# Optimization experiments

Hardware: AMD Instinct MI355X
Metric: run time of the kernel (lower is better)

The kernel has to match this reference:

```python
import jax, jax.numpy as jnp
import numpy as np

OMEGA = 10.0
SIGMA = 10.0
HID = 256
IN_DIM = 3
OUT_DIM = 3


def gabor(x, W, b):
    # torch.nn.Linear: lin = x @ W.T + b
    lin = x @ W.T + b
    # exp(1j*omega*lin - (sigma*lin)**2).real == cos(omega*lin) * exp(-(sigma*lin)**2)
    return jnp.cos(OMEGA * lin) * jnp.exp(-jnp.square(SIGMA * lin))


def _linear_init(key, out_dim, in_dim):
    kw, kb = jax.random.split(key)
    bound = 1.0 / np.sqrt(in_dim)
    W = jax.random.uniform(kw, (out_dim, in_dim), jnp.float32, -bound, bound)
    b = jax.random.uniform(kb, (out_dim,), jnp.float32, -bound, bound)
    return W, b


def setup_inputs() -> dict:
    key = jax.random.key(0)
    keys = jax.random.split(key, 7)
    N = 262144
    x = jax.random.uniform(keys[0], (N, IN_DIM), jnp.float32)
    W0, b0 = _linear_init(keys[1], HID, IN_DIM)
    W1, b1 = _linear_init(keys[2], HID, HID)
    W2, b2 = _linear_init(keys[3], HID, HID)
    W3, b3 = _linear_init(keys[4], HID, HID + IN_DIM)  # skip-concat layer
    W4, b4 = _linear_init(keys[5], HID, HID)
    Wf, bf = _linear_init(keys[6], OUT_DIM, HID)
    return {"x": x, "W0": W0, "b0": b0, "W1": W1, "b1": b1, "W2": W2,
            "b2": b2, "W3": W3, "b3": b3, "W4": W4, "b4": b4,
            "Wf": Wf, "bf": bf}


def reference(x, W0, b0, W1, b1, W2, b2, W3, b3, W4, b4, Wf, bf):
    x_in = x
    h = gabor(x, W0, b0)          # net[0]
    h = gabor(h, W1, b1)          # net[1]
    h = gabor(h, W2, b2)          # net[2]
    h = jnp.concatenate([h, x_in], axis=-1)  # skip before net[3]
    h = gabor(h, W3, b3)          # net[3]
    h = gabor(h, W4, b4)          # net[4]
    return h @ Wf.T + bf          # final linear
```

## Files before the change

### kernel.cpp

```cpp
#include <hip/hip_runtime.h>

typedef _Float16 f16x8 __attribute__((ext_vector_type(8)));
typedef _Float16 f16x4 __attribute__((ext_vector_type(4)));
typedef float    f32x4 __attribute__((ext_vector_type(4)));

#define BN    64
#define KPAD  288
#define ROWB  (KPAD * 2)
#define WELE  270336

__device__ __forceinline__ int swz(int row, int colb) {
  int c = (colb < 512) ? (colb ^ ((row & 7) << 4)) : colb;
  return row * ROWB + c;
}

__device__ __forceinline__ float gabor_f(float lin) {
  float a = 10.f * lin;
  return __cosf(a) * __expf(-a * a);
}

template <int KS>
__device__ __forceinline__ void mfma_layer(char* __restrict__ buf,
                                           const _Float16* __restrict__ Wh,
                                           const _Float16* __restrict__ Wl,
                                           const float* __restrict__ bias,
                                           int lane, int wid) {
  const int r = lane & 15;
  const int g = lane >> 4;
  const int n0 = wid * 32;
  const int x = (r & 7) << 4;

  int boff[4][2];
#pragma unroll
  for (int j = 0; j < 4; j++) {
    const int row = j * 16 + r;
    boff[j][0] = row * ROWB + ((g * 16) ^ x);
    boff[j][1] = row * ROWB + ((64 + g * 16) ^ x);
  }

  f32x4 acc[2][4];
#pragma unroll
  for (int i = 0; i < 2; i++)
#pragma unroll
    for (int j = 0; j < 4; j++) {
      f32x4 z = {0.f, 0.f, 0.f, 0.f};
      acc[i][j] = z;
    }

  const int wbase = (wid * KS) * 1024 + lane * 8;

#pragma unroll
  for (int kk = 0; kk < KS; kk++) {
    const int wof = wbase + kk * 1024;
    f16x8 a0 = *(const f16x8*)(Wh + wof);
    f16x8 a1 = *(const f16x8*)(Wh + wof + 512);
    f16x8 c0 = *(const f16x8*)(Wl + wof);
    f16x8 c1 = *(const f16x8*)(Wl + wof + 512);

    f16x8 b0, b1, b2, b3;
    if (kk < 8) {
      const int imm = (kk >> 1) * 128;
      b0 = *(const f16x8*)(buf + boff[0][kk & 1] + imm);
      b1 = *(const f16x8*)(buf + boff[1][kk & 1] + imm);
      b2 = *(const f16x8*)(buf + boff[2][kk & 1] + imm);
      b3 = *(const f16x8*)(buf + boff[3][kk & 1] + imm);
    } else {
      const int lin0 = r * ROWB + 512 + g * 16;
      b0 = *(const f16x8*)(buf + lin0);
      b1 = *(const f16x8*)(buf + lin0 + 16 * ROWB);
      b2 = *(const f16x8*)(buf + lin0 + 32 * ROWB);
      b3 = *(const f16x8*)(buf + lin0 + 48 * ROWB);
    }

    acc[0][0] = __builtin_amdgcn_mfma_f32_16x16x32_f16(a0, b0, acc[0][0], 0, 0, 0);
    acc[0][1] = __builtin_amdgcn_mfma_f32_16x16x32_f16(a0, b1, acc[0][1], 0, 0, 0);
    acc[0][2] = __builtin_amdgcn_mfma_f32_16x16x32_f16(a0, b2, acc[0][2], 0, 0, 0);
    acc[0][3] = __builtin_amdgcn_mfma_f32_16x16x32_f16(a0, b3, acc[0][3], 0, 0, 0);
    acc[1][0] = __builtin_amdgcn_mfma_f32_16x16x32_f16(a1, b0, acc[1][0], 0, 0, 0);
    acc[1][1] = __builtin_amdgcn_mfma_f32_16x16x32_f16(a1, b1, acc[1][1], 0, 0, 0);
    acc[1][2] = __builtin_amdgcn_mfma_f32_16x16x32_f16(a1, b2, acc[1][2], 0, 0, 0);
    acc[1][3] = __builtin_amdgcn_mfma_f32_16x16x32_f16(a1, b3, acc[1][3], 0, 0, 0);
    acc[0][0] = __builtin_amdgcn_mfma_f32_16x16x32_f16(c0, b0, acc[0][0], 0, 0, 0);
    acc[0][1] = __builtin_amdgcn_mfma_f32_16x16x32_f16(c0, b1, acc[0][1], 0, 0, 0);
    acc[0][2] = __builtin_amdgcn_mfma_f32_16x16x32_f16(c0, b2, acc[0][2], 0, 0, 0);
    acc[0][3] = __builtin_amdgcn_mfma_f32_16x16x32_f16(c0, b3, acc[0][3], 0, 0, 0);
    acc[1][0] = __builtin_amdgcn_mfma_f32_16x16x32_f16(c1, b0, acc[1][0], 0, 0, 0);
    acc[1][1] = __builtin_amdgcn_mfma_f32_16x16x32_f16(c1, b1, acc[1][1], 0, 0, 0);
    acc[1][2] = __builtin_amdgcn_mfma_f32_16x16x32_f16(c1, b2, acc[1][2], 0, 0, 0);
    acc[1][3] = __builtin_amdgcn_mfma_f32_16x16x32_f16(c1, b3, acc[1][3], 0, 0, 0);
  }

  __syncthreads();

#pragma unroll
  for (int i = 0; i < 2; i++) {
    const f32x4 bv = *(const f32x4*)(bias + n0 + i * 16 + g * 4);
#pragma unroll
    for (int j = 0; j < 4; j++) {
      f16x4 hv;
#pragma unroll
      for (int e = 0; e < 4; e++)
        hv[e] = (_Float16)gabor_f(acc[i][j][e] + bv[e]);
      *(f16x4*)(buf + swz(j * 16 + r, (n0 + i * 16 + g * 4) * 2)) = hv;
    }
  }

  __syncthreads();
}

extern "C" __global__ void __launch_bounds__(512, 4)
inr_fused(const float* __restrict__ x, const float* __restrict__ W0,
          const float* __restrict__ b0, const float* __restrict__ b1,
          const float* __restrict__ b2, const float* __restrict__ b3,
          const float* __restrict__ b4, const float* __restrict__ Wf,
          const float* __restrict__ bf, const _Float16* __restrict__ wsh,
          float* __restrict__ out, int npts) {
  extern __shared__ char smem[];
  char* buf = smem;

  const _Float16* w1h = wsh;
  const _Float16* w2h = wsh + 65536;
  const _Float16* w4h = wsh + 131072;
  const _Float16* w3p = wsh + 196608;
  const _Float16* w1l = wsh + WELE;
  const _Float16* w2l = wsh + WELE + 65536;
  const _Float16* w4l = wsh + WELE + 131072;
  const _Float16* w3l = wsh + WELE + 196608;

  const int tid   = threadIdx.x;
  const int pbase = blockIdx.x * BN;

  {
    const int p = tid >> 3;
    const int q = tid & 7;
    const int gp = pbase + p;
    float x0 = 0.f, x1 = 0.f, x2 = 0.f;
    if (gp < npts) {
      x0 = x[(size_t)gp * 3 + 0];
      x1 = x[(size_t)gp * 3 + 1];
      x2 = x[(size_t)gp * 3 + 2];
    }
#pragma unroll
    for (int ub = 0; ub < 32; ub += 8) {
      const int u0 = q * 32 + ub;
      f16x8 hv;
#pragma unroll
      for (int e = 0; e < 8; e++) {
        const int u = u0 + e;
        float lin = fmaf(x0, W0[u * 3 + 0],
                    fmaf(x1, W0[u * 3 + 1],
                    fmaf(x2, W0[u * 3 + 2], b0[u])));
        hv[e] = (_Float16)gabor_f(lin);
      }
      *(f16x8*)(buf + swz(p, u0 * 2)) = hv;
    }
    if (q < 4) {
      f16x8 xv = {(_Float16)0.f, (_Float16)0.f, (_Float16)0.f, (_Float16)0.f,
                  (_Float16)0.f, (_Float16)0.f, (_Float16)0.f, (_Float16)0.f};
      if (q == 0) { xv[0] = (_Float16)x0; xv[1] = (_Float16)x1; xv[2] = (_Float16)x2; }
      *(f16x8*)(buf + swz(p, (256 + q * 8) * 2)) = xv;
    }
  }
  __syncthreads();

  const int lane = tid & 63;
  const int wid  = tid >> 6;

  mfma_layer<8>(buf, w1h, w1l, b1, lane, wid);
  mfma_layer<8>(buf, w2h, w2l, b2, lane, wid);
  mfma_layer<9>(buf, w3p, w3l, b3, lane, wid);
  mfma_layer<8>(buf, w4h, w4l, b4, lane, wid);

  {
    const int p = tid >> 3;
    const int q = tid & 7;
    const int gp = pbase + p;
    const int xo = (p & 7) << 4;
    const char* rowp = buf + p * ROWB;
    float s0 = 0.f, s1 = 0.f, s2 = 0.f;
#pragma unroll
    for (int i8 = 0; i8 < 4; i8++) {
      const int ke = q * 32 + i8 * 8;
      f16x8 hv = *(const f16x8*)(rowp + ((ke * 2) ^ xo));
      const f32x4 w0a = *(const f32x4*)(Wf + 0 * 256 + ke);
      const f32x4 w0b = *(const f32x4*)(Wf + 0 * 256 + ke + 4);
      const f32x4 w1a = *(const f32x4*)(Wf + 1 * 256 + ke);
      const f32x4 w1b = *(const f32x4*)(Wf + 1 * 256 + ke + 4);
      const f32x4 w2a = *(const f32x4*)(Wf + 2 * 256 + ke);
      const f32x4 w2b = *(const f32x4*)(Wf + 2 * 256 + ke + 4);
#pragma unroll
      for (int e = 0; e < 4; e++) {
        const float ha = (float)hv[e];
        const float hb = (float)hv[e + 4];
        s0 = fmaf(ha, w0a[e], fmaf(hb, w0b[e], s0));
        s1 = fmaf(ha, w1a[e], fmaf(hb, w1b[e], s1));
        s2 = fmaf(ha, w2a[e], fmaf(hb, w2b[e], s2));
      }
    }
#pragma unroll
    for (int m = 1; m < 8; m <<= 1) {
      s0 += __shfl_xor(s0, m, 64);
      s1 += __shfl_xor(s1, m, 64);
      s2 += __shfl_xor(s2, m, 64);
    }
    if (gp < npts && q < 3) {
      const float v = (q == 0) ? (s0 + bf[0]) : ((q == 1) ? (s1 + bf[1]) : (s2 + bf[2]));
      out[(size_t)gp * 3 + q] = v;
    }
  }
}

extern "C" __global__ void conv_w(const float* __restrict__ W1,
                                  const float* __restrict__ W2,
                                  const float* __restrict__ W4,
                                  const float* __restrict__ W3,
                                  _Float16* __restrict__ wsh) {
  int idx = blockIdx.x * blockDim.x + threadIdx.x;
  if (idx >= WELE) return;

  int base, KS;
  const float* src = nullptr;
  int ldk = 256, kmax = 256;
  if (idx < 65536)       { base = 0;      KS = 8; src = W1; }
  else if (idx < 131072) { base = 65536;  KS = 8; src = W2; }
  else if (idx < 196608) { base = 131072; KS = 8; src = W4; }
  else                   { base = 196608; KS = 9; src = W3; ldk = 259; kmax = 259; }

  const int t    = idx - base;
  const int e    = t & 7;
  const int lane = (t >> 3) & 63;
  const int i    = (t >> 9) & 1;
  const int rem  = t >> 10;
  const int kk   = rem % KS;
  const int slice = rem / KS;

  const int unit = slice * 32 + i * 16 + (lane & 15);
  const int k    = kk * 32 + (lane >> 4) * 8 + e;

  const float w = (k < kmax) ? src[(size_t)unit * ldk + k] : 0.f;
  const _Float16 hi = (_Float16)w;
  const _Float16 lo = (_Float16)(w - (float)hi);
  wsh[idx] = hi;
  wsh[idx + WELE] = lo;
}

extern "C" void kernel_launch(void* const* d_in, const int* in_sizes, int n_in,
                              void* d_out, int out_size, void* d_ws, size_t ws_size,
                              hipStream_t stream) {
  const float* x  = (const float*)d_in[0];
  const float* W0 = (const float*)d_in[1];
  const float* b0 = (const float*)d_in[2];
  const float* W1 = (const float*)d_in[3];
  const float* b1 = (const float*)d_in[4];
  const float* W2 = (const float*)d_in[5];
  const float* b2 = (const float*)d_in[6];
  const float* W3 = (const float*)d_in[7];
  const float* b3 = (const float*)d_in[8];
  const float* W4 = (const float*)d_in[9];
  const float* b4 = (const float*)d_in[10];
  const float* Wf = (const float*)d_in[11];
  const float* bf = (const float*)d_in[12];
  float* out      = (float*)d_out;
  _Float16* wsh   = (_Float16*)d_ws;

  const int npts = in_sizes[0] / 3;

  conv_w<<<(WELE + 511) / 512, 512, 0, stream>>>(W1, W2, W4, W3, wsh);

  const int nblk = (npts + BN - 1) / BN;
  inr_fused<<<nblk, 512, BN * ROWB, stream>>>(x, W0, b0, b1, b2, b3, b4,
                                              Wf, bf, wsh, out, npts);
}
```

Baseline: 416.6 us.

## Double point tile to 128 per block to reuse weight fragments across more MFMAs

```diff
diff --git a/kernel.cpp b/kernel.cpp
--- a/kernel.cpp
+++ b/kernel.cpp
@@ -4,7 +4,7 @@
 typedef _Float16 f16x4 __attribute__((ext_vector_type(4)));
 typedef float    f32x4 __attribute__((ext_vector_type(4)));
 
-#define BN    64
+#define BN    128
 #define KPAD  288
 #define ROWB  (KPAD * 2)
 #define WELE  270336
@@ -30,19 +30,14 @@
   const int n0 = wid * 32;
   const int x = (r & 7) << 4;
 
-  int boff[4][2];
-#pragma unroll
-  for (int j = 0; j < 4; j++) {
-    const int row = j * 16 + r;
-    boff[j][0] = row * ROWB + ((g * 16) ^ x);
-    boff[j][1] = row * ROWB + ((64 + g * 16) ^ x);
-  }
-
-  f32x4 acc[2][4];
+  const char* bp0 = buf + r * ROWB + ((g * 16) ^ x);
+  const char* bp1 = buf + r * ROWB + (((64 + g * 16)) ^ x);
+
+  f32x4 acc[2][8];
 #pragma unroll
   for (int i = 0; i < 2; i++)
 #pragma unroll
-    for (int j = 0; j < 4; j++) {
+    for (int j = 0; j < 8; j++) {
       f32x4 z = {0.f, 0.f, 0.f, 0.f};
       acc[i][j] = z;
     }
@@ -57,37 +52,32 @@
     f16x8 c0 = *(const f16x8*)(Wl + wof);
     f16x8 c1 = *(const f16x8*)(Wl + wof + 512);
 
-    f16x8 b0, b1, b2, b3;
+    f16x8 b[8];
     if (kk < 8) {
+      const char* bp = (kk & 1) ? bp1 : bp0;
       const int imm = (kk >> 1) * 128;
-      b0 = *(const f16x8*)(buf + boff[0][kk & 1] + imm);
-      b1 = *(const f16x8*)(buf + boff[1][kk & 1] + imm);
-      b2 = *(const f16x8*)(buf + boff[2][kk & 1] + imm);
-      b3 = *(const f16x8*)(buf + boff[3][kk & 1] + imm);
+#pragma unroll
+      for (int j = 0; j < 8; j++)
+        b[j] = *(const f16x8*)(bp + j * 16 * ROWB + imm);
     } else {
-      const int lin0 = r * ROWB + 512 + g * 16;
-      b0 = *(const f16x8*)(buf + lin0);
-      b1 = *(const f16x8*)(buf + lin0 + 16 * ROWB);
-      b2 = *(const f16x8*)(buf + lin0 + 32 * ROWB);
-      b3 = *(const f16x8*)(buf + lin0 + 48 * ROWB);
-    }
-
-    acc[0][0] = __builtin_amdgcn_mfma_f32_16x16x32_f16(a0, b0, acc[0][0], 0, 0, 0);
-    acc[0][1] = __builtin_amdgcn_mfma_f32_16x16x32_f16(a0, b1, acc[0][1], 0, 0, 0);
-    acc[0][2] = __builtin_amdgcn_mfma_f32_16x16x32_f16(a0, b2, acc[0][2], 0, 0, 0);
-    acc[0][3] = __builtin_amdgcn_mfma_f32_16x16x32_f16(a0, b3, acc[0][3], 0, 0, 0);
-    acc[1][0] = __builtin_amdgcn_mfma_f32_16x16x32_f16(a1, b0, acc[1][0], 0, 0, 0);
-    acc[1][1] = __builtin_amdgcn_mfma_f32_16x16x32_f16(a1, b1, acc[1][1], 0, 0, 0);
-    acc[1][2] = __builtin_amdgcn_mfma_f32_16x16x32_f16(a1, b2, acc[1][2], 0, 0, 0);
-    acc[1][3] = __builtin_amdgcn_mfma_f32_16x16x32_f16(a1, b3, acc[1][3], 0, 0, 0);
-    acc[0][0] = __builtin_amdgcn_mfma_f32_16x16x32_f16(c0, b0, acc[0][0], 0, 0, 0);
-    acc[0][1] = __builtin_amdgcn_mfma_f32_16x16x32_f16(c0, b1, acc[0][1], 0, 0, 0);
-    acc[0][2] = __builtin_amdgcn_mfma_f32_16x16x32_f16(c0, b2, acc[0][2], 0, 0, 0);
-    acc[0][3] = __builtin_amdgcn_mfma_f32_16x16x32_f16(c0, b3, acc[0][3], 0, 0, 0);
-    acc[1][0] = __builtin_amdgcn_mfma_f32_16x16x32_f16(c1, b0, acc[1][0], 0, 0, 0);
-    acc[1][1] = __builtin_amdgcn_mfma_f32_16x16x32_f16(c1, b1, acc[1][1], 0, 0, 0);
-    acc[1][2] = __builtin_amdgcn_mfma_f32_16x16x32_f16(c1, b2, acc[1][2], 0, 0, 0);
-    acc[1][3] = __builtin_amdgcn_mfma_f32_16x16x32_f16(c1, b3, acc[1][3], 0, 0, 0);
+      const char* bp = buf + r * ROWB + 512 + g * 16;
+#pragma unroll
+      for (int j = 0; j < 8; j++)
+        b[j] = *(const f16x8*)(bp + j * 16 * ROWB);
+    }
+
+#pragma unroll
+    for (int j = 0; j < 8; j++)
+      acc[0][j] = __builtin_amdgcn_mfma_f32_16x16x32_f16(a0, b[j], acc[0][j], 0, 0, 0);
+#pragma unroll
+    for (int j = 0; j < 8; j++)
+      acc[1][j] = __builtin_amdgcn_mfma_f32_16x16x32_f16(a1, b[j], acc[1][j], 0, 0, 0);
+#pragma unroll
+    for (int j = 0; j < 8; j++)
+      acc[0][j] = __builtin_amdgcn_mfma_f32_16x16x32_f16(c0, b[j], acc[0][j], 0, 0, 0);
+#pragma unroll
+    for (int j = 0; j < 8; j++)
+      acc[1][j] = __builtin_amdgcn_mfma_f32_16x16x32_f16(c1, b[j], acc[1][j], 0, 0, 0);
   }
 
   __syncthreads();
@@ -96,7 +86,7 @@
   for (int i = 0; i < 2; i++) {
     const f32x4 bv = *(const f32x4*)(bias + n0 + i * 16 + g * 4);
 #pragma unroll
-    for (int j = 0; j < 4; j++) {
+    for (int j = 0; j < 8; j++) {
       f16x4 hv;
 #pragma unroll
       for (int e = 0; e < 4; e++)
@@ -108,7 +98,7 @@
   __syncthreads();
 }
 
-extern "C" __global__ void __launch_bounds__(512, 4)
+extern "C" __global__ void __launch_bounds__(512, 2)
 inr_fused(const float* __restrict__ x, const float* __restrict__ W0,
           const float* __restrict__ b0, const float* __restrict__ b1,
           const float* __restrict__ b2, const float* __restrict__ b3,
@@ -131,8 +121,8 @@
   const int pbase = blockIdx.x * BN;
 
   {
-    const int p = tid >> 3;
-    const int q = tid & 7;
+    const int p = tid >> 2;
+    const int q = tid & 3;
     const int gp = pbase + p;
     float x0 = 0.f, x1 = 0.f, x2 = 0.f;
     if (gp < npts) {
@@ -141,8 +131,8 @@
       x2 = x[(size_t)gp * 3 + 2];
     }
 #pragma unroll
-    for (int ub = 0; ub < 32; ub += 8) {
-      const int u0 = q * 32 + ub;
+    for (int ub = 0; ub < 64; ub += 8) {
+      const int u0 = q * 64 + ub;
       f16x8 hv;
 #pragma unroll
       for (int e = 0; e < 8; e++) {
@@ -154,7 +144,7 @@
       }
       *(f16x8*)(buf + swz(p, u0 * 2)) = hv;
     }
-    if (q < 4) {
+    {
       f16x8 xv = {(_Float16)0.f, (_Float16)0.f, (_Float16)0.f, (_Float16)0.f,
                   (_Float16)0.f, (_Float16)0.f, (_Float16)0.f, (_Float16)0.f};
       if (q == 0) { xv[0] = (_Float16)x0; xv[1] = (_Float16)x1; xv[2] = (_Float16)x2; }
@@ -172,15 +162,15 @@
   mfma_layer<8>(buf, w4h, w4l, b4, lane, wid);
 
   {
-    const int p = tid >> 3;
-    const int q = tid & 7;
+    const int p = tid >> 2;
+    const int q = tid & 3;
     const int gp = pbase + p;
     const int xo = (p & 7) << 4;
     const char* rowp = buf + p * ROWB;
     float s0 = 0.f, s1 = 0.f, s2 = 0.f;
 #pragma unroll
-    for (int i8 = 0; i8 < 4; i8++) {
-      const int ke = q * 32 + i8 * 8;
+    for (int i8 = 0; i8 < 8; i8++) {
+      const int ke = q * 64 + i8 * 8;
       f16x8 hv = *(const f16x8*)(rowp + ((ke * 2) ^ xo));
       const f32x4 w0a = *(const f32x4*)(Wf + 0 * 256 + ke);
       const f32x4 w0b = *(const f32x4*)(Wf + 0 * 256 + ke + 4);
@@ -198,7 +188,7 @@
       }
     }
 #pragma unroll
-    for (int m = 1; m < 8; m <<= 1) {
+    for (int m = 1; m < 4; m <<= 1) {
       s0 += __shfl_xor(s0, m, 64);
       s1 += __shfl_xor(s1, m, 64);
       s2 += __shfl_xor(s2, m, 64);
```

Result: slower. 499.6 us (+19.9%).
